# Kernel optimization log

Hardware: AMD Instinct MI355X
Metric: run time of the kernel (lower is better)

The kernel has to match this reference:

```python
import jax, jax.numpy as jnp
import numpy as np

N = 50000
E = 800000
IN = 128
HEADS = 4
C = 32  # out_features per head
HC = HEADS * C


def setup_inputs() -> dict:
    key = jax.random.key(0)
    ks = jax.random.split(key, 10)
    s_in = 1.0 / np.sqrt(IN)
    x = jax.random.normal(ks[0], (N, IN), dtype=jnp.float32)
    edge_index = jax.random.randint(ks[1], (2, E), 0, N, dtype=jnp.int64)
    Wq = jax.random.normal(ks[2], (IN, HC), dtype=jnp.float32) * s_in
    bq = jnp.zeros((HC,), dtype=jnp.float32)
    Wk = jax.random.normal(ks[3], (IN, HC), dtype=jnp.float32) * s_in
    bk = jnp.zeros((HC,), dtype=jnp.float32)
    Wv = jax.random.normal(ks[4], (IN, HC), dtype=jnp.float32) * s_in
    bv = jnp.zeros((HC,), dtype=jnp.float32)
    Wskip = jax.random.normal(ks[5], (IN, HC), dtype=jnp.float32) * s_in
    bskip = jnp.zeros((HC,), dtype=jnp.float32)
    return {"x": x, "edge_index": edge_index, "Wq": Wq, "bq": bq,
            "Wk": Wk, "bk": bk, "Wv": Wv, "bv": bv,
            "Wskip": Wskip, "bskip": bskip}


def reference(x, edge_index, Wq, bq, Wk, bk, Wv, bv, Wskip, bskip):
    src = edge_index[0]  # message source j
    dst = edge_index[1]  # message target i

    q = (x @ Wq + bq).reshape(N, HEADS, C)
    k = (x @ Wk + bk).reshape(N, HEADS, C)
    v = (x @ Wv + bv).reshape(N, HEADS, C)

    # per-edge attention logits: [E, H]
    logits = jnp.einsum('ehc,ehc->eh', q[dst], k[src]) / jnp.sqrt(
        jnp.asarray(C, dtype=x.dtype))

    # segment softmax over incoming edges of each target node
    seg_max = jax.ops.segment_max(logits, dst, num_segments=N)
    seg_max = jnp.where(jnp.isfinite(seg_max), seg_max, 0.0)
    expd = jnp.exp(logits - seg_max[dst])
    seg_sum = jax.ops.segment_sum(expd, dst, num_segments=N)
    alpha = expd / (seg_sum[dst] + 1e-16)  # [E, H]

    # scatter-add weighted values: [N, H, C]
    msgs = alpha[:, :, None] * v[src]
    out = jax.ops.segment_sum(msgs, dst, num_segments=N)
    out = out.reshape(N, HC) + (x @ Wskip + bskip)  # root/skip connection

    # LeakyReLU(negative_slope=0.2)
    return jnp.where(out >= 0, out, 0.2 * out)
```

## Files before the change

### kernel.cpp

```cpp
#include <hip/hip_runtime.h>

#define N_NODES 50000
#define E_EDGES 800000
#define IN_F 128
#define HC 128
#define NCOLS 512
#define ROWTILES 3125
#define SCAN_BLOCKS 196
#define PACK_BLOCKS 32
#define HIST_BLOCKS ((E_EDGES + 255) / 256)

typedef __attribute__((ext_vector_type(8))) short short8;
typedef __attribute__((ext_vector_type(4))) float floatx4;

__device__ __forceinline__ unsigned short f2bf(float f) {
    union { float f; unsigned u; } x; x.f = f;
    unsigned r = x.u + 0x7FFF + ((x.u >> 16) & 1);
    return (unsigned short)(r >> 16);
}
__device__ __forceinline__ float bflo(unsigned u) {
    union { unsigned u; float f; } c; c.u = u << 16; return c.f;
}
__device__ __forceinline__ float bfhi(unsigned u) {
    union { unsigned u; float f; } c; c.u = u & 0xFFFF0000u; return c.f;
}

__global__ __launch_bounds__(256) void pack_w(
    const float* __restrict__ Wq, const float* __restrict__ Wk,
    const float* __restrict__ Wv, const float* __restrict__ Ws,
    const float* __restrict__ bq, const float* __restrict__ bk,
    const float* __restrict__ bv, const float* __restrict__ bs,
    short* __restrict__ bpack, float* __restrict__ bcat,
    int* __restrict__ cnt)
{
    int t = blockIdx.x * 256 + threadIdx.x;
    int lane = t & 63, ks = (t >> 6) & 3, nt = t >> 8;
    int col = nt * 16 + (lane & 15);
    int sec = col >> 7, c = col & 127;
    const float* W = sec == 0 ? Wq : sec == 1 ? Wk : sec == 2 ? Wv : Ws;
    int kbase = ks * 32 + (lane >> 4) * 8;
    short8 b;
#pragma unroll
    for (int j = 0; j < 8; j++) b[j] = (short)f2bf(W[(size_t)(kbase + j) * HC + c]);
    *(short8*)(bpack + (size_t)t * 8) = b;
    if (t < NCOLS) {
        int s2 = t >> 7, c2 = t & 127;
        bcat[t] = (s2 == 0 ? bq : s2 == 1 ? bk : s2 == 2 ? bv : bs)[c2];
    }
    for (int i = t; i < N_NODES; i += PACK_BLOCKS * 256) cnt[i] = 0;
}

__global__ __launch_bounds__(256) void gemm_hist(
    const float* __restrict__ x, const short* __restrict__ bpack,
    const float* __restrict__ bcat,
    unsigned short* __restrict__ q, unsigned short* __restrict__ k,
    unsigned short* __restrict__ v, float* __restrict__ out,
    const int* __restrict__ dst, int* __restrict__ cnt, int* __restrict__ rank)
{
    if (blockIdx.x >= ROWTILES) {
        int e = (blockIdx.x - ROWTILES) * 256 + threadIdx.x;
        if (e < E_EDGES) rank[e] = atomicAdd(&cnt[dst[e]], 1);
        return;
    }
    const int rt = blockIdx.x;
    const int cg = threadIdx.x >> 6;
    const int lane = threadIdx.x & 63;
    const int m0 = rt * 16 + (lane & 15);
    const int koff = (lane >> 4) * 8;

    short8 a0[4];
#pragma unroll
    for (int ks = 0; ks < 4; ks++) {
        const float* p0 = x + (size_t)m0 * IN_F + ks * 32 + koff;
        float4 lo = *(const float4*)p0;
        float4 hi = *(const float4*)(p0 + 4);
        short8 a;
        a[0] = (short)f2bf(lo.x); a[1] = (short)f2bf(lo.y);
        a[2] = (short)f2bf(lo.z); a[3] = (short)f2bf(lo.w);
        a[4] = (short)f2bf(hi.x); a[5] = (short)f2bf(hi.y);
        a[6] = (short)f2bf(hi.z); a[7] = (short)f2bf(hi.w);
        a0[ks] = a;
    }

    unsigned short* dstb = (cg == 0) ? q : (cg == 1) ? k : v;
    const int rb0 = rt * 16 + (lane >> 4) * 4;

#pragma unroll
    for (int nt8 = 0; nt8 < 8; nt8++) {
        const int nt = cg * 8 + nt8;
        floatx4 acc = {0.f, 0.f, 0.f, 0.f};
#pragma unroll
        for (int ks = 0; ks < 4; ks++) {
            short8 b = *(const short8*)(bpack + ((size_t)(nt * 4 + ks) * 64 + lane) * 8);
            acc = __builtin_amdgcn_mfma_f32_16x16x32_bf16(a0[ks], b, acc, 0, 0, 0);
        }
        const int c = nt8 * 16 + (lane & 15);
        const float bias = bcat[cg * 128 + c];
        if (cg < 3) {
#pragma unroll
            for (int r = 0; r < 4; r++)
                dstb[(size_t)(rb0 + r) * HC + c] = f2bf(acc[r] + bias);
        } else {
#pragma unroll
            for (int r = 0; r < 4; r++)
                out[(size_t)(rb0 + r) * HC + c] = acc[r] + bias;
        }
    }
}

__global__ __launch_bounds__(256) void scan_apply(const int* __restrict__ cnt,
                                                  int* __restrict__ rowptr)
{
    __shared__ int wsum[4];
    const int t = threadIdx.x;
    const int lane = t & 63, w = t >> 6;
    const int limit = blockIdx.x * 256;

    int s = 0;
    for (int i = t; i < limit; i += 256) s += cnt[i];
#pragma unroll
    for (int off = 32; off >= 1; off >>= 1) s += __shfl_xor(s, off);
    if (lane == 0) wsum[w] = s;
    __syncthreads();
    const int prefix = wsum[0] + wsum[1] + wsum[2] + wsum[3];
    __syncthreads();

    int idx = limit + t;
    int val = (idx < N_NODES) ? cnt[idx] : 0;
    int incl = val;
#pragma unroll
    for (int off = 1; off < 64; off <<= 1) {
        int u = __shfl_up(incl, off);
        if (lane >= off) incl += u;
    }
    if (lane == 63) wsum[w] = incl;
    __syncthreads();
    int pre = 0;
#pragma unroll
    for (int i = 0; i < 4; i++) if (i < w) pre += wsum[i];
    int excl = prefix + pre + incl - val;
    if (idx < N_NODES) rowptr[idx] = excl;
    if (idx == N_NODES - 1) rowptr[N_NODES] = E_EDGES;
}

__global__ __launch_bounds__(256) void scatter_k(const int* __restrict__ src,
                                                 const int* __restrict__ dst,
                                                 const int* __restrict__ rowptr,
                                                 const int* __restrict__ rank,
                                                 int* __restrict__ ssrc)
{
    int e = blockIdx.x * 256 + threadIdx.x;
    if (e < E_EDGES) ssrc[rowptr[dst[e]] + rank[e]] = src[e];
}

__global__ __launch_bounds__(256) void node_attn(
    const unsigned short* __restrict__ q, const unsigned short* __restrict__ k,
    const unsigned short* __restrict__ v, const int* __restrict__ rowptr,
    const int* __restrict__ ssrc, float* __restrict__ out)
{
    const int wave = (blockIdx.x * 256 + threadIdx.x) >> 6;
    if (wave >= N_NODES) return;
    const int lane = threadIdx.x & 63;
    const int node = wave;
    const int g = lane >> 3;
    const int l8 = lane & 7;
    const int c0 = l8 * 16;

    const uint4 uq0 = *(const uint4*)(q + (size_t)node * HC + c0);
    const uint4 uq1 = *(const uint4*)(q + (size_t)node * HC + c0 + 8);

    float acc[16];
#pragma unroll
    for (int i = 0; i < 16; i++) acc[i] = 0.f;
    float ssum = 0.f;

    const int beg = __builtin_amdgcn_readfirstlane(rowptr[node]);
    const int end = __builtin_amdgcn_readfirstlane(rowptr[node + 1]);
    const float scale = 0.17677669529663687f;

    for (int e = beg; e < end; e += 8) {
        const int ee = e + g;
        const int jj = ssrc[ee < end ? ee : beg];
        const unsigned short* kp = k + (size_t)jj * HC + c0;
        const unsigned short* vp = v + (size_t)jj * HC + c0;
        const uint4 uk0 = *(const uint4*)kp;
        const uint4 uk1 = *(const uint4*)(kp + 8);
        const uint4 uv0 = *(const uint4*)vp;
        const uint4 uv1 = *(const uint4*)(vp + 8);

        float p = bflo(uq0.x) * bflo(uk0.x) + bfhi(uq0.x) * bfhi(uk0.x)
                + bflo(uq0.y) * bflo(uk0.y) + bfhi(uq0.y) * bfhi(uk0.y)
                + bflo(uq0.z) * bflo(uk0.z) + bfhi(uq0.z) * bfhi(uk0.z)
                + bflo(uq0.w) * bflo(uk0.w) + bfhi(uq0.w) * bfhi(uk0.w)
                + bflo(uq1.x) * bflo(uk1.x) + bfhi(uq1.x) * bfhi(uk1.x)
                + bflo(uq1.y) * bflo(uk1.y) + bfhi(uq1.y) * bfhi(uk1.y)
                + bflo(uq1.z) * bflo(uk1.z) + bfhi(uq1.z) * bfhi(uk1.z)
                + bflo(uq1.w) * bflo(uk1.w) + bfhi(uq1.w) * bfhi(uk1.w);
        p += __shfl_xor(p, 1);
        float wgt = __expf(p * scale);
        wgt = (ee < end) ? wgt : 0.f;
        ssum += wgt;

        acc[0]  += wgt * bflo(uv0.x); acc[1]  += wgt * bfhi(uv0.x);
        acc[2]  += wgt * bflo(uv0.y); acc[3]  += wgt * bfhi(uv0.y);
        acc[4]  += wgt * bflo(uv0.z); acc[5]  += wgt * bfhi(uv0.z);
        acc[6]  += wgt * bflo(uv0.w); acc[7]  += wgt * bfhi(uv0.w);
        acc[8]  += wgt * bflo(uv1.x); acc[9]  += wgt * bfhi(uv1.x);
        acc[10] += wgt * bflo(uv1.y); acc[11] += wgt * bfhi(uv1.y);
        acc[12] += wgt * bflo(uv1.z); acc[13] += wgt * bfhi(uv1.z);
        acc[14] += wgt * bflo(uv1.w); acc[15] += wgt * bfhi(uv1.w);
    }

    ssum += __shfl_xor(ssum, 8);
    ssum += __shfl_xor(ssum, 16);
    ssum += __shfl_xor(ssum, 32);
#pragma unroll
    for (int i = 0; i < 16; i++) {
        acc[i] += __shfl_xor(acc[i], 8);
        acc[i] += __shfl_xor(acc[i], 16);
        acc[i] += __shfl_xor(acc[i], 32);
    }

    if (g == 0) {
        const float inv = 1.0f / (ssum + 1e-16f);
        float* op = out + (size_t)node * HC + c0;
        float o[16];
#pragma unroll
        for (int i = 0; i < 16; i += 4) {
            float4 s = *(const float4*)(op + i);
            o[i]     = acc[i]     * inv + s.x;
            o[i + 1] = acc[i + 1] * inv + s.y;
            o[i + 2] = acc[i + 2] * inv + s.z;
            o[i + 3] = acc[i + 3] * inv + s.w;
        }
#pragma unroll
        for (int i = 0; i < 16; i++) o[i] = o[i] >= 0.f ? o[i] : 0.2f * o[i];
#pragma unroll
        for (int i = 0; i < 16; i += 4)
            *(float4*)(op + i) = make_float4(o[i], o[i + 1], o[i + 2], o[i + 3]);
    }
}

extern "C" void kernel_launch(void* const* d_in, const int* in_sizes, int n_in,
                              void* d_out, int out_size, void* d_ws, size_t ws_size,
                              hipStream_t stream)
{
    const float* x    = (const float*)d_in[0];
    const int*   ei   = (const int*)d_in[1];
    const float* Wq   = (const float*)d_in[2];
    const float* bq   = (const float*)d_in[3];
    const float* Wk   = (const float*)d_in[4];
    const float* bk   = (const float*)d_in[5];
    const float* Wv   = (const float*)d_in[6];
    const float* bv   = (const float*)d_in[7];
    const float* Wsk  = (const float*)d_in[8];
    const float* bsk  = (const float*)d_in[9];
    float* out = (float*)d_out;

    char* w = (char*)d_ws;
    const size_t NFB = (size_t)N_NODES * HC * sizeof(unsigned short);
    unsigned short* q = (unsigned short*)w;            w += NFB;
    unsigned short* k = (unsigned short*)w;            w += NFB;
    unsigned short* v = (unsigned short*)w;            w += NFB;
    short* bpack = (short*)w;                          w += 8192 * 8 * sizeof(short);
    float* bcat  = (float*)w;                          w += NCOLS * sizeof(float);
    int* cnt    = (int*)w;                             w += N_NODES * sizeof(int);
    int* rowptr = (int*)w;                             w += (N_NODES + 1) * sizeof(int);
    int* rank   = (int*)w;                             w += (size_t)E_EDGES * sizeof(int);
    int* ssrc   = (int*)w;

    const int* srcIdx = ei;
    const int* dstIdx = ei + E_EDGES;

    pack_w<<<PACK_BLOCKS, 256, 0, stream>>>(Wq, Wk, Wv, Wsk, bq, bk, bv, bsk,
                                            bpack, bcat, cnt);
    gemm_hist<<<ROWTILES + HIST_BLOCKS, 256, 0, stream>>>(
        x, bpack, bcat, q, k, v, out, dstIdx, cnt, rank);
    scan_apply<<<SCAN_BLOCKS, 256, 0, stream>>>(cnt, rowptr);
    scatter_k<<<(E_EDGES + 255) / 256, 256, 0, stream>>>(srcIdx, dstIdx, rowptr, rank, ssrc);
    node_attn<<<(N_NODES * 64) / 256, 256, 0, stream>>>(q, k, v, rowptr, ssrc, out);
}
```

Baseline: 174.5 us.

## Persistent GEMM with register-resident weights, LDS-staged stores, and per-head edge gather

Measured after the change: 195.6 us. 1.12x slower.

```diff
diff --git a/kernel.cpp b/kernel.cpp
--- a/kernel.cpp
+++ b/kernel.cpp
@@ -4,11 +4,10 @@
 #define E_EDGES 800000
 #define IN_F 128
 #define HC 128
-#define NCOLS 512
 #define ROWTILES 3125
+#define GEMM_BLOCKS 500
+#define HIST_BLOCKS 1563
 #define SCAN_BLOCKS 196
-#define PACK_BLOCKS 32
-#define HIST_BLOCKS ((E_EDGES + 255) / 256)
 
 typedef __attribute__((ext_vector_type(8))) short short8;
 typedef __attribute__((ext_vector_type(4))) float floatx4;
@@ -25,85 +24,106 @@
     union { unsigned u; float f; } c; c.u = u & 0xFFFF0000u; return c.f;
 }
 
-__global__ __launch_bounds__(256) void pack_w(
+__global__ __launch_bounds__(512) void gemm_hist(
+    const float* __restrict__ x,
     const float* __restrict__ Wq, const float* __restrict__ Wk,
     const float* __restrict__ Wv, const float* __restrict__ Ws,
     const float* __restrict__ bq, const float* __restrict__ bk,
     const float* __restrict__ bv, const float* __restrict__ bs,
-    short* __restrict__ bpack, float* __restrict__ bcat,
-    int* __restrict__ cnt)
-{
-    int t = blockIdx.x * 256 + threadIdx.x;
-    int lane = t & 63, ks = (t >> 6) & 3, nt = t >> 8;
-    int col = nt * 16 + (lane & 15);
-    int sec = col >> 7, c = col & 127;
-    const float* W = sec == 0 ? Wq : sec == 1 ? Wk : sec == 2 ? Wv : Ws;
-    int kbase = ks * 32 + (lane >> 4) * 8;
-    short8 b;
-#pragma unroll
-    for (int j = 0; j < 8; j++) b[j] = (short)f2bf(W[(size_t)(kbase + j) * HC + c]);
-    *(short8*)(bpack + (size_t)t * 8) = b;
-    if (t < NCOLS) {
-        int s2 = t >> 7, c2 = t & 127;
-        bcat[t] = (s2 == 0 ? bq : s2 == 1 ? bk : s2 == 2 ? bv : bs)[c2];
-    }
-    for (int i = t; i < N_NODES; i += PACK_BLOCKS * 256) cnt[i] = 0;
-}
-
-__global__ __launch_bounds__(256) void gemm_hist(
-    const float* __restrict__ x, const short* __restrict__ bpack,
-    const float* __restrict__ bcat,
     unsigned short* __restrict__ q, unsigned short* __restrict__ k,
     unsigned short* __restrict__ v, float* __restrict__ out,
     const int* __restrict__ dst, int* __restrict__ cnt, int* __restrict__ rank)
 {
-    if (blockIdx.x >= ROWTILES) {
-        int e = (blockIdx.x - ROWTILES) * 256 + threadIdx.x;
+    if (blockIdx.x >= GEMM_BLOCKS) {
+        int e = (blockIdx.x - GEMM_BLOCKS) * 512 + threadIdx.x;
         if (e < E_EDGES) rank[e] = atomicAdd(&cnt[dst[e]], 1);
         return;
     }
-    const int rt = blockIdx.x;
-    const int cg = threadIdx.x >> 6;
-    const int lane = threadIdx.x & 63;
-    const int m0 = rt * 16 + (lane & 15);
-    const int koff = (lane >> 4) * 8;
-
-    short8 a0[4];
-#pragma unroll
-    for (int ks = 0; ks < 4; ks++) {
-        const float* p0 = x + (size_t)m0 * IN_F + ks * 32 + koff;
-        float4 lo = *(const float4*)p0;
-        float4 hi = *(const float4*)(p0 + 4);
-        short8 a;
-        a[0] = (short)f2bf(lo.x); a[1] = (short)f2bf(lo.y);
-        a[2] = (short)f2bf(lo.z); a[3] = (short)f2bf(lo.w);
-        a[4] = (short)f2bf(hi.x); a[5] = (short)f2bf(hi.y);
-        a[6] = (short)f2bf(hi.z); a[7] = (short)f2bf(hi.w);
-        a0[ks] = a;
-    }
-
-    unsigned short* dstb = (cg == 0) ? q : (cg == 1) ? k : v;
-    const int rb0 = rt * 16 + (lane >> 4) * 4;
-
-#pragma unroll
-    for (int nt8 = 0; nt8 < 8; nt8++) {
-        const int nt = cg * 8 + nt8;
-        floatx4 acc = {0.f, 0.f, 0.f, 0.f};
+    __shared__ float As[16][132];
+    __shared__ unsigned short Ep[3][16][136];
+
+    const int tid = threadIdx.x;
+    const int wv = tid >> 6;
+    const int lane = tid & 63;
+    const int cg = wv >> 1, hf = wv & 1;
+    const int l16 = lane & 15, kh = lane >> 4;
+
+    const float* Wsec = cg == 0 ? Wq : cg == 1 ? Wk : cg == 2 ? Wv : Ws;
+    const float* bsec = cg == 0 ? bq : cg == 1 ? bk : cg == 2 ? bv : bs;
+
+    short8 breg[4][4];
+    float bias_[4];
+#pragma unroll
+    for (int n = 0; n < 4; n++) {
+        const int col = (hf * 4 + n) * 16 + l16;
+        bias_[n] = bsec[col];
 #pragma unroll
         for (int ks = 0; ks < 4; ks++) {
-            short8 b = *(const short8*)(bpack + ((size_t)(nt * 4 + ks) * 64 + lane) * 8);
-            acc = __builtin_amdgcn_mfma_f32_16x16x32_bf16(a0[ks], b, acc, 0, 0, 0);
-        }
-        const int c = nt8 * 16 + (lane & 15);
-        const float bias = bcat[cg * 128 + c];
+            short8 bb;
+#pragma unroll
+            for (int j = 0; j < 8; j++)
+                bb[j] = (short)f2bf(Wsec[(size_t)(ks * 32 + kh * 8 + j) * HC + col]);
+            breg[n][ks] = bb;
+        }
+    }
+
+    for (int rt = blockIdx.x; rt < ROWTILES; rt += GEMM_BLOCKS) {
+        __syncthreads();
+        {
+            int r = tid >> 5, c4 = (tid & 31) * 4;
+            float4 xv = *(const float4*)(x + (size_t)(rt * 16 + r) * IN_F + c4);
+            *(float4*)&As[r][c4] = xv;
+        }
+        __syncthreads();
+
+        short8 a[4];
+#pragma unroll
+        for (int ks = 0; ks < 4; ks++) {
+            const float* ap = &As[l16][ks * 32 + kh * 8];
+            float4 lo = *(const float4*)ap;
+            float4 hi = *(const float4*)(ap + 4);
+            short8 aa;
+            aa[0] = (short)f2bf(lo.x); aa[1] = (short)f2bf(lo.y);
+            aa[2] = (short)f2bf(lo.z); aa[3] = (short)f2bf(lo.w);
+            aa[4] = (short)f2bf(hi.x); aa[5] = (short)f2bf(hi.y);
+            aa[6] = (short)f2bf(hi.z); aa[7] = (short)f2bf(hi.w);
+            a[ks] = aa;
+        }
+
+        floatx4 acc[4];
+#pragma unroll
+        for (int n = 0; n < 4; n++) acc[n] = {0.f, 0.f, 0.f, 0.f};
+#pragma unroll
+        for (int ks = 0; ks < 4; ks++)
+#pragma unroll
+            for (int n = 0; n < 4; n++)
+                acc[n] = __builtin_amdgcn_mfma_f32_16x16x32_bf16(a[ks], breg[n][ks], acc[n], 0, 0, 0);
+
         if (cg < 3) {
 #pragma unroll
-            for (int r = 0; r < 4; r++)
-                dstb[(size_t)(rb0 + r) * HC + c] = f2bf(acc[r] + bias);
+            for (int n = 0; n < 4; n++) {
+                const int c = (hf * 4 + n) * 16 + l16;
+#pragma unroll
+                for (int r = 0; r < 4; r++)
+                    Ep[cg][kh * 4 + r][c] = f2bf(acc[n][r] + bias_[n]);
+            }
         } else {
 #pragma unroll
-            for (int r = 0; r < 4; r++)
-                out[(size_t)(rb0 + r) * HC + c] = acc[r] + bias;
+            for (int n = 0; n < 4; n++) {
+                const int c = (hf * 4 + n) * 16 + l16;
+#pragma unroll
+                for (int r = 0; r < 4; r++)
+                    out[(size_t)(rt * 16 + kh * 4 + r) * HC + c] = acc[n][r] + bias_[n];
+            }
+        }
+        __syncthreads();
+        for (int i = tid; i < 768; i += 512) {
+            int cgi = i >> 8, wi = i & 255;
+            int r = wi >> 4, cb = (wi & 15) * 8;
+            uint4 val = *(const uint4*)&Ep[cgi][r][cb];
+            unsigned short* dp = (cgi == 0 ? q : cgi == 1 ? k : v)
+                                 + (size_t)(rt * 16 + r) * HC + cb;
+            *(uint4*)dp = val;
         }
     }
 }
@@ -162,82 +182,80 @@
     if (wave >= N_NODES) return;
     const int lane = threadIdx.x & 63;
     const int node = wave;
-    const int g = lane >> 3;
-    const int l8 = lane & 7;
-    const int c0 = l8 * 16;
-
-    const uint4 uq0 = *(const uint4*)(q + (size_t)node * HC + c0);
-    const uint4 uq1 = *(const uint4*)(q + (size_t)node * HC + c0 + 8);
-
-    float acc[16];
-#pragma unroll
-    for (int i = 0; i < 16; i++) acc[i] = 0.f;
+    const int g = lane >> 2;
+    const int h = lane & 3;
+    const int c0 = h * 32;
+
+    uint4 uq[4];
+#pragma unroll
+    for (int w = 0; w < 4; w++)
+        uq[w] = *(const uint4*)(q + (size_t)node * HC + c0 + w * 8);
+
+    float acc[32];
+#pragma unroll
+    for (int i = 0; i < 32; i++) acc[i] = 0.f;
     float ssum = 0.f;
 
     const int beg = __builtin_amdgcn_readfirstlane(rowptr[node]);
     const int end = __builtin_amdgcn_readfirstlane(rowptr[node + 1]);
     const float scale = 0.17677669529663687f;
 
-    for (int e = beg; e < end; e += 8) {
+    for (int e = beg; e < end; e += 16) {
         const int ee = e + g;
         const int jj = ssrc[ee < end ? ee : beg];
         const unsigned short* kp = k + (size_t)jj * HC + c0;
         const unsigned short* vp = v + (size_t)jj * HC + c0;
-        const uint4 uk0 = *(const uint4*)kp;
-        const uint4 uk1 = *(const uint4*)(kp + 8);
-        const uint4 uv0 = *(const uint4*)vp;
-        const uint4 uv1 = *(const uint4*)(vp + 8);
-
-        float p = bflo(uq0.x) * bflo(uk0.x) + bfhi(uq0.x) * bfhi(uk0.x)
-                + bflo(uq0.y) * bflo(uk0.y) + bfhi(uq0.y) * bfhi(uk0.y)
-                + bflo(uq0.z) * bflo(uk0.z) + bfhi(uq0.z) * bfhi(uk0.z)
-                + bflo(uq0.w) * bflo(uk0.w) + bfhi(uq0.w) * bfhi(uk0.w)
-                + bflo(uq1.x) * bflo(uk1.x) + bfhi(uq1.x) * bfhi(uk1.x)
-                + bflo(uq1.y) * bflo(uk1.y) + bfhi(uq1.y) * bfhi(uk1.y)
-                + bflo(uq1.z) * bflo(uk1.z) + bfhi(uq1.z) * bfhi(uk1.z)
-                + bflo(uq1.w) * bflo(uk1.w) + bfhi(uq1.w) * bfhi(uk1.w);
-        p += __shfl_xor(p, 1);
+        uint4 uk[4], uv[4];
+#pragma unroll
+        for (int w = 0; w < 4; w++) uk[w] = *(const uint4*)(kp + w * 8);
+#pragma unroll
+        for (int w = 0; w < 4; w++) uv[w] = *(const uint4*)(vp + w * 8);
+
+        float p = 0.f;
+#pragma unroll
+        for (int w = 0; w < 4; w++) {
+            p += bflo(uq[w].x) * bflo(uk[w].x) + bfhi(uq[w].x) * bfhi(uk[w].x);
+            p += bflo(uq[w].y) * bflo(uk[w].y) + bfhi(uq[w].y) * bfhi(uk[w].y);
+            p += bflo(uq[w].z) * bflo(uk[w].z) + bfhi(uq[w].z) * bfhi(uk[w].z);
+            p += bflo(uq[w].w) * bflo(uk[w].w) + bfhi(uq[w].w) * bfhi(uk[w].w);
+        }
         float wgt = __expf(p * scale);
         wgt = (ee < end) ? wgt : 0.f;
         ssum += wgt;
-
-        acc[0]  += wgt * bflo(uv0.x); acc[1]  += wgt * bfhi(uv0.x);
-        acc[2]  += wgt * bflo(uv0.y); acc[3]  += wgt * bfhi(uv0.y);
-        acc[4]  += wgt * bflo(uv0.z); acc[5]  += wgt * bfhi(uv0.z);
-        acc[6]  += wgt * bflo(uv0.w); acc[7]  += wgt * bfhi(uv0.w);
-        acc[8]  += wgt * bflo(uv1.x); acc[9]  += wgt * bfhi(uv1.x);
-        acc[10] += wgt * bflo(uv1.y); acc[11] += wgt * bfhi(uv1.y);
-        acc[12] += wgt * bflo(uv1.z); acc[13] += wgt * bfhi(uv1.z);
-        acc[14] += wgt * bflo(uv1.w); acc[15] += wgt * bfhi(uv1.w);
-    }
-
+#pragma unroll
+        for (int w = 0; w < 4; w++) {
+            acc[w * 8 + 0] += wgt * bflo(uv[w].x); acc[w * 8 + 1] += wgt * bfhi(uv[w].x);
+            acc[w * 8 + 2] += wgt * bflo(uv[w].y); acc[w * 8 + 3] += wgt * bfhi(uv[w].y);
+            acc[w * 8 + 4] += wgt * bflo(uv[w].z); acc[w * 8 + 5] += wgt * bfhi(uv[w].z);
+            acc[w * 8 + 6] += wgt * bflo(uv[w].w); acc[w * 8 + 7] += wgt * bfhi(uv[w].w);
+        }
+    }
+
+    ssum += __shfl_xor(ssum, 4);
     ssum += __shfl_xor(ssum, 8);
     ssum += __shfl_xor(ssum, 16);
     ssum += __shfl_xor(ssum, 32);
 #pragma unroll
-    for (int i = 0; i < 16; i++) {
+    for (int i = 0; i < 32; i++) {
+        acc[i] += __shfl_xor(acc[i], 4);
         acc[i] += __shfl_xor(acc[i], 8);
         acc[i] += __shfl_xor(acc[i], 16);
         acc[i] += __shfl_xor(acc[i], 32);
     }
 
-    if (g == 0) {
+    if (g < 8) {
         const float inv = 1.0f / (ssum + 1e-16f);
-        float* op = out + (size_t)node * HC + c0;
-        float o[16];
-#pragma unroll
-        for (int i = 0; i < 16; i += 4) {
-            float4 s = *(const float4*)(op + i);
-            o[i]     = acc[i]     * inv + s.x;
-            o[i + 1] = acc[i + 1] * inv + s.y;
-            o[i + 2] = acc[i + 2] * inv + s.z;
-            o[i + 3] = acc[i + 3] * inv + s.w;
-        }
-#pragma unroll
-        for (int i = 0; i < 16; i++) o[i] = o[i] >= 0.f ? o[i] : 0.2f * o[i];
-#pragma unroll
-        for (int i = 0; i < 16; i += 4)
-            *(float4*)(op + i) = make_float4(o[i], o[i + 1], o[i + 2], o[i + 3]);
+        float* op = out + (size_t)node * HC + c0 + g * 4;
+        float4 s = *(const float4*)op;
+        float o0 = acc[g * 4 + 0] * inv + s.x;
+        float o1 = acc[g * 4 + 1] * inv + s.y;
+        float o2 = acc[g * 4 + 2] * inv + s.z;
+        float o3 = acc[g * 4 + 3] * inv + s.w;
+        o0 = o0 >= 0.f ? o0 : 0.2f * o0;
+        o1 = o1 >= 0.f ? o1 : 0.2f * o1;
+        o2 = o2 >= 0.f ? o2 : 0.2f * o2;
+        o3 = o3 >= 0.f ? o3 : 0.2f * o3;
+        *(float4*)op = make_float4(o0, o1, o2, o3);
     }
 }
 
@@ -262,8 +280,6 @@
     unsigned short* q = (unsigned short*)w;            w += NFB;
     unsigned short* k = (unsigned short*)w;            w += NFB;
     unsigned short* v = (unsigned short*)w;            w += NFB;
-    short* bpack = (short*)w;                          w += 8192 * 8 * sizeof(short);
-    float* bcat  = (float*)w;                          w += NCOLS * sizeof(float);
     int* cnt    = (int*)w;                             w += N_NODES * sizeof(int);
     int* rowptr = (int*)w;                             w += (N_NODES + 1) * sizeof(int);
     int* rank   = (int*)w;                             w += (size_t)E_EDGES * sizeof(int);
@@ -272,10 +288,9 @@
     const int* srcIdx = ei;
     const int* dstIdx = ei + E_EDGES;
 
-    pack_w<<<PACK_BLOCKS, 256, 0, stream>>>(Wq, Wk, Wv, Wsk, bq, bk, bv, bsk,
-                                            bpack, bcat, cnt);
-    gemm_hist<<<ROWTILES + HIST_BLOCKS, 256, 0, stream>>>(
-        x, bpack, bcat, q, k, v, out, dstIdx, cnt, rank);
+    hipMemsetAsync(cnt, 0, N_NODES * sizeof(int), stream);
+    gemm_hist<<<GEMM_BLOCKS + HIST_BLOCKS, 512, 0, stream>>>(
+        x, Wq, Wk, Wv, Wsk, bq, bk, bv, bsk, q, k, v, out, dstIdx, cnt, rank);
     scan_apply<<<SCAN_BLOCKS, 256, 0, stream>>>(cnt, rowptr);
     scatter_k<<<(E_EDGES + 255) / 256, 256, 0, stream>>>(srcIdx, dstIdx, rowptr, rank, ssrc);
     node_attn<<<(N_NODES * 64) / 256, 256, 0, stream>>>(q, k, v, rowptr, ssrc, out);
```
